# Kernel optimization log

Hardware: AMD Instinct MI355X
Metric: run time of the kernel (lower is better)

The kernel has to match this reference:

```python
import jax, jax.numpy as jnp
import numpy as np

MARGIN = 1.0

def setup_inputs() -> dict:
    key = jax.random.key(0)
    k1, k2 = jax.random.split(key)
    B, C = 65536, 1000
    pred = jax.random.normal(k1, (B, C), dtype=jnp.float32)
    target = jax.random.randint(k2, (B,), 0, C, dtype=jnp.int64)
    return {"pred": pred, "target": target}

def reference(pred, target):
    # pred: [B, C], target: [B]
    B, C = pred.shape
    correct = jnp.take_along_axis(pred, target[:, None], axis=1)  # [B, 1]
    margins = pred - correct + MARGIN                              # [B, C]
    # exclude the true class (its margin would be exactly MARGIN)
    is_target = jnp.arange(C)[None, :] == target[:, None]
    margins = jnp.where(is_target, -jnp.inf, margins)
    # per-sample hinge: max(0, max_{j != y} margins)
    per_sample = jnp.maximum(jnp.max(margins, axis=1), 0.0)        # [B]
    return jnp.mean(per_sample)
```

## Files before the change

### kernel.cpp

```cpp
#include <hip/hip_runtime.h>
#include <hip/hip_bf16.h>
#include <math.h>

#define BLOCK 256
#define WAVES_PER_BLOCK (BLOCK / 64)
#define GRID1 2048

__global__ __launch_bounds__(BLOCK) void hinge_rows_kernel(
    const float* __restrict__ pred, const int* __restrict__ target,
    float* __restrict__ partial, int B, int C) {
  const int lane = threadIdx.x & 63;
  const int wave = threadIdx.x >> 6;
  const int gwave = blockIdx.x * WAVES_PER_BLOCK + wave;
  const int nwaves = gridDim.x * WAVES_PER_BLOCK;
  const int nvec = C >> 2;

  float sum = 0.0f;

  for (int row = gwave; row < B; row += nwaves) {
    const float* rp = pred + (size_t)row * (size_t)C;
    const int y = target[row];
    const float correct = rp[y];

    float m = -INFINITY;
    const float4* rp4 = (const float4*)rp;
    for (int i = lane; i < nvec; i += 64) {
      float4 v = rp4[i];
      const int base = i << 2;
      v.x = (base + 0 == y) ? -INFINITY : v.x;
      v.y = (base + 1 == y) ? -INFINITY : v.y;
      v.z = (base + 2 == y) ? -INFINITY : v.z;
      v.w = (base + 3 == y) ? -INFINITY : v.w;
      m = fmaxf(m, fmaxf(fmaxf(v.x, v.y), fmaxf(v.z, v.w)));
    }
    for (int c = (nvec << 2) + lane; c < C; c += 64) {
      if (c != y) m = fmaxf(m, rp[c]);
    }

    #pragma unroll
    for (int off = 32; off; off >>= 1)
      m = fmaxf(m, __shfl_xor(m, off));

    sum += fmaxf(m - correct + 1.0f, 0.0f);
  }

  __shared__ float lsum[WAVES_PER_BLOCK];
  if (lane == 0) lsum[wave] = sum;
  __syncthreads();
  if (threadIdx.x == 0) {
    float s = 0.0f;
    #pragma unroll
    for (int w = 0; w < WAVES_PER_BLOCK; ++w) s += lsum[w];
    partial[blockIdx.x] = s;
  }
}

__global__ __launch_bounds__(BLOCK) void hinge_reduce_kernel(
    const float* __restrict__ partial, int n, float* __restrict__ out,
    float scale) {
  float s = 0.0f;
  for (int i = threadIdx.x; i < n; i += BLOCK) s += partial[i];

  #pragma unroll
  for (int off = 32; off; off >>= 1) s += __shfl_xor(s, off);

  const int lane = threadIdx.x & 63;
  const int wave = threadIdx.x >> 6;
  __shared__ float lsum[WAVES_PER_BLOCK];
  if (lane == 0) lsum[wave] = s;
  __syncthreads();
  if (threadIdx.x == 0) {
    float t = 0.0f;
    #pragma unroll
    for (int w = 0; w < WAVES_PER_BLOCK; ++w) t += lsum[w];
    out[0] = t * scale;
  }
}

extern "C" void kernel_launch(void* const* d_in, const int* in_sizes, int n_in,
                              void* d_out, int out_size, void* d_ws, size_t ws_size,
                              hipStream_t stream) {
  const float* pred = (const float*)d_in[0];
  const int* target = (const int*)d_in[1];
  float* out = (float*)d_out;
  float* partial = (float*)d_ws;

  const int B = in_sizes[1];
  const int C = in_sizes[0] / B;

  hinge_rows_kernel<<<GRID1, BLOCK, 0, stream>>>(pred, target, partial, B, C);
  hinge_reduce_kernel<<<1, BLOCK, 0, stream>>>(partial, GRID1, out, 1.0f / (float)B);
}
```

Before: 352.0 us.

## Assign contiguous row chunks per wave, prefetch targets, use nontemporal loads

Each wave now handles a contiguous block of rows instead of a grid-strided set. It preloads every row's target index and correct-class value in parallel across lanes, then broadcasts them with shuffles. This removes the serial dependent target/correct load chain at the start of each row. The inner row loop uses nontemporal vector loads with unroll 4 to cut cache pollution and raise memory-level parallelism. The preload assumes rows per wave is at most 64; with larger B, rows past lane 63 would read garbage via the shuffle.

```diff
diff --git a/kernel.cpp b/kernel.cpp
--- a/kernel.cpp
+++ b/kernel.cpp
@@ -6,6 +6,8 @@
 #define WAVES_PER_BLOCK (BLOCK / 64)
 #define GRID1 2048
 
+typedef float f32x4 __attribute__((ext_vector_type(4)));
+
 __global__ __launch_bounds__(BLOCK) void hinge_rows_kernel(
     const float* __restrict__ pred, const int* __restrict__ target,
     float* __restrict__ partial, int B, int C) {
@@ -13,24 +15,37 @@
   const int wave = threadIdx.x >> 6;
   const int gwave = blockIdx.x * WAVES_PER_BLOCK + wave;
   const int nwaves = gridDim.x * WAVES_PER_BLOCK;
+  const int rpw = (B + nwaves - 1) / nwaves;
+  const int base = gwave * rpw;
   const int nvec = C >> 2;
+
+  int ty = 0;
+  float corr = 0.0f;
+  if (lane < rpw && base + lane < B) {
+    ty = target[base + lane];
+    corr = pred[(size_t)(base + lane) * (size_t)C + ty];
+  }
 
   float sum = 0.0f;
 
-  for (int row = gwave; row < B; row += nwaves) {
+  for (int k = 0; k < rpw; ++k) {
+    const int row = base + k;
+    if (row >= B) break;
+    const int y = __shfl(ty, k);
+    const float correct = __shfl(corr, k);
+
     const float* rp = pred + (size_t)row * (size_t)C;
-    const int y = target[row];
-    const float correct = rp[y];
+    const f32x4* rp4 = (const f32x4*)rp;
 
     float m = -INFINITY;
-    const float4* rp4 = (const float4*)rp;
+    #pragma unroll 4
     for (int i = lane; i < nvec; i += 64) {
-      float4 v = rp4[i];
-      const int base = i << 2;
-      v.x = (base + 0 == y) ? -INFINITY : v.x;
-      v.y = (base + 1 == y) ? -INFINITY : v.y;
-      v.z = (base + 2 == y) ? -INFINITY : v.z;
-      v.w = (base + 3 == y) ? -INFINITY : v.w;
+      f32x4 v = __builtin_nontemporal_load(&rp4[i]);
+      const int b0 = i << 2;
+      v.x = (b0 + 0 == y) ? -INFINITY : v.x;
+      v.y = (b0 + 1 == y) ? -INFINITY : v.y;
+      v.z = (b0 + 2 == y) ? -INFINITY : v.z;
+      v.w = (b0 + 3 == y) ? -INFINITY : v.w;
       m = fmaxf(m, fmaxf(fmaxf(v.x, v.y), fmaxf(v.z, v.w)));
     }
     for (int c = (nvec << 2) + lane; c < C; c += 64) {
```

After: 349.9 us. No clear change (-0.6%).
